# Performance work log

Hardware: AMD Instinct MI355X
Metric: run time of the kernel (lower is better)

Reference implementation:

```python
import jax, jax.numpy as jnp
import numpy as np

NUM_HEADS = 8
EPS = 1e-6


def setup_inputs() -> dict:
    key = jax.random.key(0)
    ks = jax.random.split(key, 6)
    B, T, E = 2, 4096, 512
    s = 0.02
    x = jax.random.normal(ks[0], (B, T, E), dtype=jnp.float32)
    Wq = jax.random.normal(ks[1], (E, E), dtype=jnp.float32) * s
    Wk = jax.random.normal(ks[2], (E, E), dtype=jnp.float32) * s
    Wv = jax.random.normal(ks[3], (E, E), dtype=jnp.float32) * s
    Wo = jax.random.normal(ks[4], (E, E), dtype=jnp.float32) * s
    bq = jnp.zeros((E,), jnp.float32)
    bk = jnp.zeros((E,), jnp.float32)
    bv = jnp.zeros((E,), jnp.float32)
    bo = jnp.zeros((E,), jnp.float32)
    return {"x": x, "Wq": Wq, "bq": bq, "Wk": Wk, "bk": bk,
            "Wv": Wv, "bv": bv, "Wo": Wo, "bo": bo}


def _linear(x, W, b):
    # torch nn.Linear: y = x @ W.T + b
    return x @ W.T + b


def _feature_map(x):
    return jax.nn.elu(x) + 1.0


def _linear_attention(x, Wq, bq, Wk, bk, Wv, bv, Wo, bo):
    B, T, E = x.shape
    H = NUM_HEADS
    D = E // H

    def heads(y):  # (B,T,E) -> (T,B,H,D), time-major for scan
        return y.reshape(B, T, H, D).transpose(1, 0, 2, 3)

    q = _feature_map(heads(_linear(x, Wq, bq)))
    k = _feature_map(heads(_linear(x, Wk, bk)))
    v = heads(_linear(x, Wv, bv))

    # Causal linear attention: running KV outer-product state S (B,H,D,D)
    # and running key sum z (B,H,D). Equivalent to the naive
    # cumsum-of-outer-products (B,H,T,D,D) formulation, but O(D^2) state.
    S0 = jnp.zeros((B, H, D, D), x.dtype)
    z0 = jnp.zeros((B, H, D), x.dtype)

    def step(carry, qkv):
        S, z = carry
        qt, kt, vt = qkv  # each (B,H,D)
        S = S + kt[..., :, None] * vt[..., None, :]
        z = z + kt
        num = jnp.einsum('bhd,bhde->bhe', qt, S)
        den = jnp.sum(qt * z, axis=-1) + EPS  # (B,H)
        return (S, z), num / den[..., None]

    _, out = jax.lax.scan(step, (S0, z0), (q, k, v))  # (T,B,H,D)
    out = out.transpose(1, 0, 2, 3).reshape(B, T, E)
    return _linear(out, Wo, bo)


def reference(x, Wq, bq, Wk, bk, Wv, bv, Wo, bo):
    return _linear_attention(x, Wq, bq, Wk, bk, Wv, bv, Wo, bo)
```

## Files before the change

kernel.cpp:

```cpp
#include <hip/hip_runtime.h>
#include <hip/hip_bf16.h>

#define T_SEQ 4096
#define EMB   512
#define NH    8
#define HD    64
#define BATCH 2
#define M_ROWS (BATCH * T_SEQ)
#define NCHUNK 64
#define CS     64
#define BHEADS (BATCH * NH)

using bf16 = __hip_bfloat16;
typedef __attribute__((ext_vector_type(8))) short short8;
typedef __attribute__((ext_vector_type(4))) short short4v;
typedef __attribute__((ext_vector_type(4))) float floatx4;

__device__ __forceinline__ float bs2f(short s) {
    return __uint_as_float(((unsigned)(unsigned short)s) << 16);
}
__device__ __forceinline__ short f2bs(float f) {
    bf16 h = __float2bfloat16(f);
    return *reinterpret_cast<short*>(&h);
}
__device__ __forceinline__ float load_elem(const bf16* p, size_t i) {
    return __bfloat162float(p[i]);
}
__device__ __forceinline__ void stage8(const bf16* g, short* l) {
    *reinterpret_cast<short8*>(l) = *reinterpret_cast<const short8*>(g);
}
__device__ __forceinline__ void stage8(const float* g, short* l) {
    float4 a = *reinterpret_cast<const float4*>(g);
    float4 b = *reinterpret_cast<const float4*>(g + 4);
    short8 v;
    v[0] = f2bs(a.x); v[1] = f2bs(a.y); v[2] = f2bs(a.z); v[3] = f2bs(a.w);
    v[4] = f2bs(b.x); v[5] = f2bs(b.y); v[6] = f2bs(b.z); v[7] = f2bs(b.w);
    *reinterpret_cast<short8*>(l) = v;
}

__device__ __forceinline__ void gload_lds16(const short* g, short* l) {
    __builtin_amdgcn_global_load_lds(
        (const __attribute__((address_space(1))) void*)g,
        (__attribute__((address_space(3))) void*)l, 16, 0, 0);
}

#define LDSTR 72

__device__ __forceinline__ int probe_mode(const void* x) {
    const uint4* p = (const uint4*)x;
    const int tid = threadIdx.x;
    bool bad = false;
    #pragma unroll
    for (int i = 0; i < 2; ++i) {
        uint4 u = p[tid + i * 256];
        const unsigned w[4] = {u.x, u.y, u.z, u.w};
        #pragma unroll
        for (int k = 0; k < 4; ++k) {
            const float f = __uint_as_float(w[k] << 16);
            if (!(fabsf(f) <= 1e9f)) bad = true;
        }
    }
    return __syncthreads_or(bad ? 1 : 0) ? 1 : 0;
}

template <typename T>
__device__ __forceinline__ void convert_body(
    const void* const* in, short* xb, short* Wb, short* bb, int c)
{
    if (c < 524288) {
        stage8((const T*)in[0] + (size_t)c * 8, xb + (size_t)c * 8);
    } else if (c < 655360) {
        const int c2 = c - 524288;
        const int w = c2 >> 15;
        const int off = (c2 & 32767) * 8;
        const T* src = (const T*)in[w == 0 ? 1 : (w == 1 ? 3 : (w == 2 ? 5 : 7))];
        stage8(src + off, Wb + w * 262144 + off);
    } else if (c < 655616) {
        const int c3 = c - 655360;
        const int bsel = c3 >> 6;
        const int off = (c3 & 63) * 8;
        const T* src = (const T*)in[bsel == 0 ? 2 : (bsel == 1 ? 4 : (bsel == 2 ? 6 : 8))];
        stage8(src + off, bb + bsel * 512 + off);
    }
}

__global__ __launch_bounds__(256) void convert_all(
    const void* x, const void* Wq, const void* bq,
    const void* Wk, const void* bk, const void* Wv, const void* bv,
    const void* Wo, const void* bo,
    short* __restrict__ xb, short* __restrict__ Wb, short* __restrict__ bb)
{
    const void* in[9] = {x, Wq, bq, Wk, bk, Wv, bv, Wo, bo};
    const int mode = probe_mode(x);
    const int c = blockIdx.x * 256 + threadIdx.x;
    if (mode) convert_body<float>(in, xb, Wb, bb, c);
    else      convert_body<bf16>(in, xb, Wb, bb, c);
}

__global__ __launch_bounds__(256) void qkv_gemm_dl(
    const short* __restrict__ xb, const short* __restrict__ Wb,
    const short* __restrict__ bb,
    bf16* __restrict__ Qf, bf16* __restrict__ Kf, bf16* __restrict__ Vf)
{
    const int mtile = blockIdx.x;
    const int ntile = blockIdx.y;
    const int which = ntile >> 2;
    const short* W = Wb + (size_t)which * 262144;
    const bf16* bias = (const bf16*)(bb + which * 512);
    bf16* outp = (which == 0) ? Qf : ((which == 1) ? Kf : Vf);
    const int nbase = (ntile & 3) * 128;
    const int mbase = mtile * 128;

    __shared__ short As[128 * 64];
    __shared__ short Bs[128 * 64];

    const int tid  = threadIdx.x;
    const int wave = tid >> 6, lane = tid & 63;
    const int wm = wave >> 1, wn = wave & 1;
    const int lm = lane & 15, quad = lane >> 4;
    const int srow = lane >> 3;
    const int scol = (lane & 7) * 8;

    floatx4 acc[4][4];
    const floatx4 zero = {0.f, 0.f, 0.f, 0.f};
    #pragma unroll
    for (int mt = 0; mt < 4; ++mt)
        #pragma unroll
        for (int nt = 0; nt < 4; ++nt) acc[mt][nt] = zero;

    for (int kt = 0; kt < EMB; kt += 64) {
        #pragma unroll
        for (int j = 0; j < 4; ++j) {
            const int issue = wave * 4 + j;
            const int row = issue * 8 + srow;
            gload_lds16(xb + (size_t)(mbase + row) * EMB + kt + scol,
                        &As[issue * 512]);
            gload_lds16(W  + (size_t)(nbase + row) * EMB + kt + scol,
                        &Bs[issue * 512]);
        }
        __syncthreads();
        #pragma unroll
        for (int ks = 0; ks < 2; ++ks) {
            short8 af[4], bfr[4];
            #pragma unroll
            for (int mt = 0; mt < 4; ++mt)
                af[mt] = *reinterpret_cast<const short8*>(
                    &As[(wm * 64 + mt * 16 + lm) * 64 + ks * 32 + quad * 8]);
            #pragma unroll
            for (int nt = 0; nt < 4; ++nt)
                bfr[nt] = *reinterpret_cast<const short8*>(
                    &Bs[(wn * 64 + nt * 16 + lm) * 64 + ks * 32 + quad * 8]);
            #pragma unroll
            for (int mt = 0; mt < 4; ++mt)
                #pragma unroll
                for (int nt = 0; nt < 4; ++nt)
                    acc[mt][nt] = __builtin_amdgcn_mfma_f32_16x16x32_bf16(
                        af[mt], bfr[nt], acc[mt][nt], 0, 0, 0);
        }
        __syncthreads();
    }

    #pragma unroll
    for (int nt = 0; nt < 4; ++nt) {
        const int col = nbase + wn * 64 + nt * 16 + lm;
        const float bv_ = load_elem(bias, col & 511);
        const int h = col >> 6, d = col & 63;
        #pragma unroll
        for (int mt = 0; mt < 4; ++mt)
            #pragma unroll
            for (int r = 0; r < 4; ++r) {
                const int row = mbase + wm * 64 + mt * 16 + quad * 4 + r;
                const int b = row >> 12, t = row & (T_SEQ - 1);
                float v = acc[mt][nt][r] + bv_;
                if (which != 2) v = (v > 0.f) ? (v + 1.f) : __expf(v);
                outp[(((size_t)(b * NH + h)) * T_SEQ + t) * HD + d] = __float2bfloat16(v);
            }
    }
}

__global__ __launch_bounds__(256) void chunk_kv(
    const bf16* __restrict__ Kf, const bf16* __restrict__ Vf,
    float* __restrict__ KVt, float* __restrict__ ksum)
{
    const int bh = blockIdx.x >> 6;
    const int c  = blockIdx.x & 63;
    __shared__ short Kt[64 * LDSTR];
    __shared__ short Vt[64 * LDSTR];
    const int tid = threadIdx.x;
    const bf16* kp = Kf + ((size_t)bh * T_SEQ + c * CS) * HD;
    const bf16* vp = Vf + ((size_t)bh * T_SEQ + c * CS) * HD;

    #pragma unroll
    for (int j = 0; j < 2; ++j) {
        const int u = j * 256 + tid;
        const int e0 = u * 8;
        const int s = e0 >> 6, d0 = e0 & 63;
        short8 ku = *reinterpret_cast<const short8*>(kp + e0);
        short8 vu = *reinterpret_cast<const short8*>(vp + e0);
        #pragma unroll
        for (int i = 0; i < 8; ++i) {
            Kt[(d0 + i) * LDSTR + s] = ku[i];
            Vt[(d0 + i) * LDSTR + s] = vu[i];
        }
    }
    __syncthreads();

    const int w = tid >> 6, lane = tid & 63;
    const int lm = lane & 15, quad = lane >> 4;

    floatx4 acc[4];
    const floatx4 zero = {0.f, 0.f, 0.f, 0.f};
    #pragma unroll
    for (int nt = 0; nt < 4; ++nt) acc[nt] = zero;

    #pragma unroll
    for (int ks = 0; ks < 2; ++ks) {
        short8 av = *reinterpret_cast<const short8*>(
            &Vt[(w * 16 + lm) * LDSTR + ks * 32 + quad * 8]);
        #pragma unroll
        for (int nt = 0; nt < 4; ++nt) {
            short8 bk = *reinterpret_cast<const short8*>(
                &Kt[(nt * 16 + lm) * LDSTR + ks * 32 + quad * 8]);
            acc[nt] = __builtin_amdgcn_mfma_f32_16x16x32_bf16(av, bk, acc[nt], 0, 0, 0);
        }
    }

    float* kvout = KVt + ((size_t)bh * NCHUNK + c) * 4096;
    #pragma unroll
    for (int nt = 0; nt < 4; ++nt)
        #pragma unroll
        for (int r = 0; r < 4; ++r) {
            const int dv = w * 16 + quad * 4 + r;
            const int dk = nt * 16 + lm;
            kvout[dv * 64 + dk] = acc[nt][r];
        }

    if (tid < 64) {
        float s = 0.f;
        #pragma unroll 8
        for (int t = 0; t < 64; ++t) s += bs2f(Kt[tid * LDSTR + t]);
        ksum[((size_t)bh * NCHUNK + c) * 64 + tid] = s;
    }
}

__global__ __launch_bounds__(256) void prefix_kv(
    float* __restrict__ KVt, float* __restrict__ ksum)
{
    const int bh   = blockIdx.x >> 4;
    const int part = blockIdx.x & 15;
    const int tid  = threadIdx.x;
    const int e    = part * 256 + tid;
    float* base = KVt + (size_t)bh * NCHUNK * 4096 + e;

    float s = 0.f;
    #pragma unroll
    for (int cb = 0; cb < 4; ++cb) {
        float v[16];
        #pragma unroll
        for (int i = 0; i < 16; ++i) v[i] = base[(size_t)(cb * 16 + i) * 4096];
        #pragma unroll
        for (int i = 0; i < 16; ++i) {
            const float tmp = v[i];
            base[(size_t)(cb * 16 + i) * 4096] = s;
            s += tmp;
        }
    }

    if (part == 0 && tid < 64) {
        float* zb = ksum + (size_t)bh * NCHUNK * 64 + tid;
        float z = 0.f;
        #pragma unroll
        for (int cb = 0; cb < 4; ++cb) {
            float v[16];
            #pragma unroll
            for (int i = 0; i < 16; ++i) v[i] = zb[(size_t)(cb * 16 + i) * 64];
            #pragma unroll
            for (int i = 0; i < 16; ++i) {
                const float tmp = v[i];
                zb[(size_t)(cb * 16 + i) * 64] = z;
                z += tmp;
            }
        }
    }
}

__global__ __launch_bounds__(256) void attn_mfma(
    const bf16* __restrict__ Qf, const bf16* __restrict__ Kf,
    const bf16* __restrict__ Vf, const float* __restrict__ KVt,
    const float* __restrict__ ksum, bf16* __restrict__ Of)
{
    const int bh = blockIdx.x >> 6;
    const int c  = blockIdx.x & 63;
    const int b  = bh >> 3, h = bh & 7;

    __shared__ short Qs [64 * LDSTR];
    __shared__ short Ksn[64 * LDSTR];
    __shared__ short Vt [64 * LDSTR];
    __shared__ short Ps [64 * LDSTR];
    __shared__ short St [64 * LDSTR];
    __shared__ float zprev[64];

    const int tid = threadIdx.x;
    const int w = tid >> 6, lane = tid & 63;
    const int lm = lane & 15, quad = lane >> 4;
    const size_t coff = ((size_t)bh * T_SEQ + c * CS) * HD;
    const float* Sp = KVt + ((size_t)bh * NCHUNK + c) * 4096;

    #pragma unroll
    for (int j = 0; j < 2; ++j) {
        const int u  = j * 256 + tid;
        const int e0 = u * 8;
        const int r = e0 >> 6, cc = e0 & 63;
        *reinterpret_cast<short8*>(&Qs [r * LDSTR + cc]) =
            *reinterpret_cast<const short8*>(Qf + coff + e0);
        *reinterpret_cast<short8*>(&Ksn[r * LDSTR + cc]) =
            *reinterpret_cast<const short8*>(Kf + coff + e0);
        short8 vu = *reinterpret_cast<const short8*>(Vf + coff + e0);
        #pragma unroll
        for (int i = 0; i < 8; ++i) Vt[(cc + i) * LDSTR + r] = vu[i];
    }
    #pragma unroll
    for (int j = 0; j < 4; ++j) {
        const int u  = j * 256 + tid;
        const int dv = u >> 4, d0 = (u & 15) * 4;
        const float4 s4 = reinterpret_cast<const float4*>(Sp)[u];
        short4v pk;
        pk[0] = f2bs(s4.x); pk[1] = f2bs(s4.y);
        pk[2] = f2bs(s4.z); pk[3] = f2bs(s4.w);
        *reinterpret_cast<short4v*>(&St[dv * LDSTR + d0]) = pk;
    }
    if (tid < 64) zprev[tid] = ksum[((size_t)bh * NCHUNK + c) * 64 + tid];
    __syncthreads();

    const floatx4 zero = {0.f, 0.f, 0.f, 0.f};
    short8 aq[2];
    #pragma unroll
    for (int ks = 0; ks < 2; ++ks)
        aq[ks] = *reinterpret_cast<const short8*>(
            &Qs[(w * 16 + lm) * LDSTR + ks * 32 + quad * 8]);

    floatx4 pacc[4];
    #pragma unroll
    for (int nt = 0; nt < 4; ++nt) pacc[nt] = zero;
    #pragma unroll
    for (int ks = 0; ks < 2; ++ks)
        #pragma unroll
        for (int nt = 0; nt < 4; ++nt) {
            short8 bk = *reinterpret_cast<const short8*>(
                &Ksn[(nt * 16 + lm) * LDSTR + ks * 32 + quad * 8]);
            pacc[nt] = __builtin_amdgcn_mfma_f32_16x16x32_bf16(aq[ks], bk, pacc[nt], 0, 0, 0);
        }

    float tot[4] = {0.f, 0.f, 0.f, 0.f};
    #pragma unroll
    for (int nt = 0; nt < 4; ++nt)
        #pragma unroll
        for (int r = 0; r < 4; ++r) {
            const int t = w * 16 + quad * 4 + r;
            const int s = nt * 16 + lm;
            const float m = (s <= t) ? pacc[nt][r] : 0.f;
            Ps[t * LDSTR + s] = f2bs(m);
            tot[r] += m;
        }
    #pragma unroll
    for (int r = 0; r < 4; ++r) {
        const int t = w * 16 + quad * 4 + r;
        #pragma unroll
        for (int j = 0; j < 4; ++j) {
            const int d = lm + j * 16;
            tot[r] += bs2f(Qs[t * LDSTR + d]) * zprev[d];
        }
    }
    #pragma unroll
    for (int mask = 1; mask < 16; mask <<= 1)
        #pragma unroll
        for (int r = 0; r < 4; ++r) tot[r] += __shfl_xor(tot[r], mask);
    float rdenl[4];
    #pragma unroll
    for (int r = 0; r < 4; ++r) rdenl[r] = 1.f / (tot[r] + 1e-6f);

    floatx4 oacc[4];
    #pragma unroll
    for (int nt = 0; nt < 4; ++nt) oacc[nt] = zero;
    #pragma unroll
    for (int ks = 0; ks < 2; ++ks)
        #pragma unroll
        for (int nt = 0; nt < 4; ++nt) {
            short8 bs = *reinterpret_cast<const short8*>(
                &St[(nt * 16 + lm) * LDSTR + ks * 32 + quad * 8]);
            oacc[nt] = __builtin_amdgcn_mfma_f32_16x16x32_bf16(aq[ks], bs, oacc[nt], 0, 0, 0);
        }
    __syncthreads();

    #pragma unroll
    for (int ks = 0; ks < 2; ++ks) {
        short8 ap = *reinterpret_cast<const short8*>(
            &Ps[(w * 16 + lm) * LDSTR + ks * 32 + quad * 8]);
        #pragma unroll
        for (int nt = 0; nt < 4; ++nt) {
            short8 bv = *reinterpret_cast<const short8*>(
                &Vt[(nt * 16 + lm) * LDSTR + ks * 32 + quad * 8]);
            oacc[nt] = __builtin_amdgcn_mfma_f32_16x16x32_bf16(ap, bv, oacc[nt], 0, 0, 0);
        }
    }

    #pragma unroll
    for (int nt = 0; nt < 4; ++nt)
        #pragma unroll
        for (int r = 0; r < 4; ++r) {
            const int t  = w * 16 + quad * 4 + r;
            const int dv = nt * 16 + lm;
            const int tg = c * CS + t;
            Of[((size_t)(b * T_SEQ + tg)) * EMB + h * HD + dv] =
                __float2bfloat16(oacc[nt][r] * rdenl[r]);
        }
}

__global__ __launch_bounds__(256) void out_proj_dl(
    const void* __restrict__ xprobe,
    const short* __restrict__ A, const short* __restrict__ Wb,
    const short* __restrict__ bb, void* __restrict__ out)
{
    const int mode = probe_mode(xprobe);

    const int mbase = blockIdx.x * 128;
    const int nbase = blockIdx.y * 128;
    const short* W = Wb + (size_t)3 * 262144;
    const bf16* bias = (const bf16*)(bb + 3 * 512);

    __shared__ short As[128 * 64];
    __shared__ short Bs[128 * 64];

    const int tid  = threadIdx.x;
    const int wave = tid >> 6, lane = tid & 63;
    const int wm = wave >> 1, wn = wave & 1;
    const int lm = lane & 15, quad = lane >> 4;
    const int srow = lane >> 3;
    const int scol = (lane & 7) * 8;

    floatx4 acc[4][4];
    const floatx4 zero = {0.f, 0.f, 0.f, 0.f};
    #pragma unroll
    for (int mt = 0; mt < 4; ++mt)
        #pragma unroll
        for (int nt = 0; nt < 4; ++nt) acc[mt][nt] = zero;

    for (int kt = 0; kt < EMB; kt += 64) {
        #pragma unroll
        for (int j = 0; j < 4; ++j) {
            const int issue = wave * 4 + j;
            const int row = issue * 8 + srow;
            gload_lds16(A + (size_t)(mbase + row) * EMB + kt + scol,
                        &As[issue * 512]);
            gload_lds16(W + (size_t)(nbase + row) * EMB + kt + scol,
                        &Bs[issue * 512]);
        }
        __syncthreads();
        #pragma unroll
        for (int ks = 0; ks < 2; ++ks) {
            short8 af[4], bfr[4];
            #pragma unroll
            for (int mt = 0; mt < 4; ++mt)
                af[mt] = *reinterpret_cast<const short8*>(
                    &As[(wm * 64 + mt * 16 + lm) * 64 + ks * 32 + quad * 8]);
            #pragma unroll
            for (int nt = 0; nt < 4; ++nt)
                bfr[nt] = *reinterpret_cast<const short8*>(
                    &Bs[(wn * 64 + nt * 16 + lm) * 64 + ks * 32 + quad * 8]);
            #pragma unroll
            for (int mt = 0; mt < 4; ++mt)
                #pragma unroll
                for (int nt = 0; nt < 4; ++nt)
                    acc[mt][nt] = __builtin_amdgcn_mfma_f32_16x16x32_bf16(
                        af[mt], bfr[nt], acc[mt][nt], 0, 0, 0);
        }
        __syncthreads();
    }

    #pragma unroll
    for (int nt = 0; nt < 4; ++nt) {
        const int col = nbase + wn * 64 + nt * 16 + lm;
        const float bv_ = load_elem(bias, col);
        #pragma unroll
        for (int mt = 0; mt < 4; ++mt)
            #pragma unroll
            for (int r = 0; r < 4; ++r) {
                const int row = mbase + wm * 64 + mt * 16 + quad * 4 + r;
                const float v = acc[mt][nt][r] + bv_;
                if (mode) ((float*)out)[(size_t)row * EMB + col] = v;
                else      ((bf16*)out)[(size_t)row * EMB + col] = __float2bfloat16(v);
            }
    }
}

extern "C" void kernel_launch(void* const* d_in, const int* in_sizes, int n_in,
                              void* d_out, int out_size, void* d_ws, size_t ws_size,
                              hipStream_t stream)
{
    bf16* Qf = (bf16*)((char*)d_ws + 64);
    bf16* Kf = Qf + 4194304;
    bf16* Vf = Kf + 4194304;
    float* KVt = (float*)(Vf + 4194304);
    short* xb = (short*)KVt;
    float* ks = KVt + 4194304;
    bf16* Of = (bf16*)(ks + 65536);
    short* Wb = (short*)(Of + 4194304);
    short* bb = Wb + 1048576;

    convert_all<<<dim3(2561), 256, 0, stream>>>(
        d_in[0], d_in[1], d_in[2], d_in[3], d_in[4],
        d_in[5], d_in[6], d_in[7], d_in[8], xb, Wb, bb);

    qkv_gemm_dl<<<dim3(64, 12), 256, 0, stream>>>(xb, Wb, bb, Qf, Kf, Vf);
    chunk_kv<<<dim3(BHEADS * NCHUNK), 256, 0, stream>>>(Kf, Vf, KVt, ks);
    prefix_kv<<<dim3(BHEADS * 16), 256, 0, stream>>>(KVt, ks);
    attn_mfma<<<dim3(BHEADS * NCHUNK), 256, 0, stream>>>(Qf, Kf, Vf, KVt, ks, Of);

    out_proj_dl<<<dim3(64, 4), 256, 0, stream>>>(
        d_in[0], (const short*)Of, Wb, bb, d_out);
}
```

Before: 159.3 us.

## Emit bf16 prefix KV state and read it directly from global in attention

prefix_kv now writes the exclusive prefix-summed KV state as bf16 into a separate buffer instead of overwriting the fp32 buffer in place. It also loads all 64 chunk values up front before scanning. attn_mfma then reads the bf16 state straight from global memory as MFMA operands, which removes the St LDS tile, the fp32-to-bf16 staging loop and one __syncthreads, and it adds a min-blocks hint of 4. This halves the state traffic read by attention and lowers LDS use, at the cost of uncoalesced-ish global operand loads and higher register pressure in prefix_kv.

```diff
diff --git a/kernel.cpp b/kernel.cpp
--- a/kernel.cpp
+++ b/kernel.cpp
@@ -13,7 +13,6 @@
 
 using bf16 = __hip_bfloat16;
 typedef __attribute__((ext_vector_type(8))) short short8;
-typedef __attribute__((ext_vector_type(4))) short short4v;
 typedef __attribute__((ext_vector_type(4))) float floatx4;
 
 __device__ __forceinline__ float bs2f(short s) {
@@ -244,49 +243,43 @@
 }
 
 __global__ __launch_bounds__(256) void prefix_kv(
-    float* __restrict__ KVt, float* __restrict__ ksum)
+    const float* __restrict__ KVt, bf16* __restrict__ KVb,
+    float* __restrict__ ksum)
 {
     const int bh   = blockIdx.x >> 4;
     const int part = blockIdx.x & 15;
     const int tid  = threadIdx.x;
     const int e    = part * 256 + tid;
-    float* base = KVt + (size_t)bh * NCHUNK * 4096 + e;
-
+    const float* src = KVt + (size_t)bh * NCHUNK * 4096 + e;
+    bf16* dst = KVb + (size_t)bh * NCHUNK * 4096 + e;
+
+    float v[64];
+    #pragma unroll
+    for (int i = 0; i < 64; ++i) v[i] = src[(size_t)i * 4096];
     float s = 0.f;
     #pragma unroll
-    for (int cb = 0; cb < 4; ++cb) {
-        float v[16];
-        #pragma unroll
-        for (int i = 0; i < 16; ++i) v[i] = base[(size_t)(cb * 16 + i) * 4096];
-        #pragma unroll
-        for (int i = 0; i < 16; ++i) {
-            const float tmp = v[i];
-            base[(size_t)(cb * 16 + i) * 4096] = s;
-            s += tmp;
-        }
+    for (int i = 0; i < 64; ++i) {
+        dst[(size_t)i * 4096] = __float2bfloat16(s);
+        s += v[i];
     }
 
     if (part == 0 && tid < 64) {
         float* zb = ksum + (size_t)bh * NCHUNK * 64 + tid;
         float z = 0.f;
-        #pragma unroll
-        for (int cb = 0; cb < 4; ++cb) {
-            float v[16];
-            #pragma unroll
-            for (int i = 0; i < 16; ++i) v[i] = zb[(size_t)(cb * 16 + i) * 64];
-            #pragma unroll
-            for (int i = 0; i < 16; ++i) {
-                const float tmp = v[i];
-                zb[(size_t)(cb * 16 + i) * 64] = z;
-                z += tmp;
-            }
-        }
-    }
-}
-
-__global__ __launch_bounds__(256) void attn_mfma(
+        float zv[64];
+        #pragma unroll
+        for (int i = 0; i < 64; ++i) zv[i] = zb[(size_t)i * 64];
+        #pragma unroll
+        for (int i = 0; i < 64; ++i) {
+            zb[(size_t)i * 64] = z;
+            z += zv[i];
+        }
+    }
+}
+
+__global__ __launch_bounds__(256, 4) void attn_mfma(
     const bf16* __restrict__ Qf, const bf16* __restrict__ Kf,
-    const bf16* __restrict__ Vf, const float* __restrict__ KVt,
+    const bf16* __restrict__ Vf, const bf16* __restrict__ KVb,
     const float* __restrict__ ksum, bf16* __restrict__ Of)
 {
     const int bh = blockIdx.x >> 6;
@@ -297,14 +290,13 @@
     __shared__ short Ksn[64 * LDSTR];
     __shared__ short Vt [64 * LDSTR];
     __shared__ short Ps [64 * LDSTR];
-    __shared__ short St [64 * LDSTR];
     __shared__ float zprev[64];
 
     const int tid = threadIdx.x;
     const int w = tid >> 6, lane = tid & 63;
     const int lm = lane & 15, quad = lane >> 4;
     const size_t coff = ((size_t)bh * T_SEQ + c * CS) * HD;
-    const float* Sp = KVt + ((size_t)bh * NCHUNK + c) * 4096;
+    const bf16* Sb = KVb + ((size_t)bh * NCHUNK + c) * 4096;
 
     #pragma unroll
     for (int j = 0; j < 2; ++j) {
@@ -319,16 +311,6 @@
         #pragma unroll
         for (int i = 0; i < 8; ++i) Vt[(cc + i) * LDSTR + r] = vu[i];
     }
-    #pragma unroll
-    for (int j = 0; j < 4; ++j) {
-        const int u  = j * 256 + tid;
-        const int dv = u >> 4, d0 = (u & 15) * 4;
-        const float4 s4 = reinterpret_cast<const float4*>(Sp)[u];
-        short4v pk;
-        pk[0] = f2bs(s4.x); pk[1] = f2bs(s4.y);
-        pk[2] = f2bs(s4.z); pk[3] = f2bs(s4.w);
-        *reinterpret_cast<short4v*>(&St[dv * LDSTR + d0]) = pk;
-    }
     if (tid < 64) zprev[tid] = ksum[((size_t)bh * NCHUNK + c) * 64 + tid];
     __syncthreads();
 
@@ -387,10 +369,9 @@
         #pragma unroll
         for (int nt = 0; nt < 4; ++nt) {
             short8 bs = *reinterpret_cast<const short8*>(
-                &St[(nt * 16 + lm) * LDSTR + ks * 32 + quad * 8]);
+                Sb + (nt * 16 + lm) * 64 + ks * 32 + quad * 8);
             oacc[nt] = __builtin_amdgcn_mfma_f32_16x16x32_bf16(aq[ks], bs, oacc[nt], 0, 0, 0);
         }
-    __syncthreads();
 
     #pragma unroll
     for (int ks = 0; ks < 2; ++ks) {
@@ -506,6 +487,7 @@
     bf16* Of = (bf16*)(ks + 65536);
     short* Wb = (short*)(Of + 4194304);
     short* bb = Wb + 1048576;
+    bf16* KVb = (bf16*)(bb + 2048);
 
     convert_all<<<dim3(2561), 256, 0, stream>>>(
         d_in[0], d_in[1], d_in[2], d_in[3], d_in[4],
@@ -513,8 +495,8 @@
 
     qkv_gemm_dl<<<dim3(64, 12), 256, 0, stream>>>(xb, Wb, bb, Qf, Kf, Vf);
     chunk_kv<<<dim3(BHEADS * NCHUNK), 256, 0, stream>>>(Kf, Vf, KVt, ks);
-    prefix_kv<<<dim3(BHEADS * 16), 256, 0, stream>>>(KVt, ks);
-    attn_mfma<<<dim3(BHEADS * NCHUNK), 256, 0, stream>>>(Qf, Kf, Vf, KVt, ks, Of);
+    prefix_kv<<<dim3(BHEADS * 16), 256, 0, stream>>>(KVt, KVb, ks);
+    attn_mfma<<<dim3(BHEADS * NCHUNK), 256, 0, stream>>>(Qf, Kf, Vf, KVb, ks, Of);
 
     out_proj_dl<<<dim3(64, 4), 256, 0, stream>>>(
         d_in[0], (const short*)Of, Wb, bb, d_out);
```

Result: no change. 161.1 us (+1.1%).
